# Kernel optimization log

Hardware: AMD Instinct MI355X
Metric: run time of the kernel (lower is better)

The kernel has to match this reference:

```python
import jax, jax.numpy as jnp
import numpy as np

EPS_LN = 1e-12
EPS_COS = 1e-8
B, L, H, S = 64, 512, 768, 32


def _layernorm(x, gamma, beta):
    mu = jnp.mean(x, axis=-1, keepdims=True)
    var = jnp.mean(jnp.square(x - mu), axis=-1, keepdims=True)
    return (x - mu) * jax.lax.rsqrt(var + EPS_LN) * gamma + beta


def setup_inputs() -> dict:
    key = jax.random.key(0)
    k = jax.random.split(key, 8)
    hidden_states = jax.random.normal(k[0], (B, L, H), dtype=jnp.float32)
    glyph_pooled = jax.random.normal(k[1], (B * S, H), dtype=jnp.float32)
    W = jax.random.normal(k[2], (H, H), dtype=jnp.float32) * (1.0 / np.sqrt(H))
    b = jnp.zeros((H,), dtype=jnp.float32)
    g1 = jnp.ones((H,), dtype=jnp.float32)
    b1 = jnp.zeros((H,), dtype=jnp.float32)
    g2 = jnp.ones((H,), dtype=jnp.float32)
    b2 = jnp.zeros((H,), dtype=jnp.float32)
    start = jax.random.randint(k[3], (B,), 0, 256, dtype=jnp.int64 if jax.config.jax_enable_x64 else jnp.int32)
    length = jax.random.randint(k[4], (B,), 1, 129, dtype=start.dtype)
    end = jnp.minimum(start + length, L)
    return {"hidden_states": hidden_states, "glyph_pooled": glyph_pooled, "W": W, "b": b,
            "g1": g1, "b1": b1, "g2": g2, "b2": b2, "glyph_start": start, "glyph_end": end}


def reference(hidden_states, glyph_pooled, W, b, g1, b1, g2, b2, glyph_start, glyph_end):
    # transform: Linear + LayerNorm on pooled glyph encoder output, then (b s) h -> b s h
    t = glyph_pooled @ W.T + b                         # [B*S, H]
    glyph_out = _layernorm(t, g1, b1).reshape(B, S, H)  # [B, S, H]

    # ragged mean pooling: mean over hidden_states[i, start[i]:end[i]] via mask
    pos = jnp.arange(L)[None, :]                        # [1, L]
    mask = (pos >= glyph_start[:, None]) & (pos < glyph_end[:, None])  # [B, L]
    maskf = mask.astype(hidden_states.dtype)
    count = jnp.maximum(jnp.sum(maskf, axis=1, keepdims=True), 1.0)    # [B, 1]
    seg_mean = jnp.einsum('bl,blh->bh', maskf, hidden_states) / count  # [B, H]

    sel = _layernorm(seg_mean, g2, b2)[:, None, :]      # [B, 1, H], broadcast over S

    # cosine similarity along last dim (torch default eps=1e-8)
    num = jnp.sum(sel * glyph_out, axis=-1)             # [B, S]
    nx = jnp.linalg.norm(sel, axis=-1)                  # [B, 1]
    ny = jnp.linalg.norm(glyph_out, axis=-1)            # [B, S]
    score = num / jnp.maximum(nx * ny, EPS_COS)
    return score
```

## Files before the change

kernel.cpp:

```cpp
#include <hip/hip_runtime.h>
#include <hip/hip_bf16.h>
#include <math.h>

#define BB 64
#define LL 512
#define HH 768
#define SS 32
#define MM 2048
#define EPS_LN 1e-12f
#define EPS_COS 1e-8f

#define NKS 12
#define NGB 384
#define CH_PER_G (NKS * 2 * 64)
#define A_RG (MM / 16)
#define B_RG (HH / 16)
#define LDST 772
#define SEG_SLICES 8
#define SEG_BLK (BB * SEG_SLICES)

#define SCALE_X 4096.0f
#define SCALE_W 131072.0f
#define INV_SC  1.8626451e-9f

typedef __attribute__((ext_vector_type(4))) int int4v;
typedef __attribute__((ext_vector_type(4))) float f32x4;

static __device__ inline void quant(float x, float scale,
                                    signed char& hi, signed char& lo) {
    int v = (int)rintf(x * scale);
    v = max(-32639, min(32639, v));
    const signed char l8 = (signed char)(v & 0xFF);
    hi = (signed char)((v - (int)l8) >> 8);
    lo = l8;
}

__global__ __launch_bounds__(256) void k_prep(
    const float* __restrict__ gp, const float* __restrict__ Wm,
    const float* __restrict__ hs,
    const int* __restrict__ gstart, const int* __restrict__ gend,
    int4v* __restrict__ a_ws, int4v* __restrict__ b_ws,
    float* __restrict__ pp)
{
    __shared__ __align__(16) float xs[16][LDST];
    const int bid = blockIdx.x;
    const int t = threadIdx.x;

    if (bid < SEG_BLK) {
        const int b = bid >> 3;
        const int sl = bid & 7;
        const int s0 = gstart[b], e0 = gend[b];
        const int lo = max(s0, sl * 64);
        const int hi = min(e0, sl * 64 + 64);
        const float* base = hs + (size_t)b * LL * HH;
        const int c0 = t, c1 = t + 256, c2 = t + 512;
        float a[3][4];
#pragma unroll
        for (int j = 0; j < 3; ++j)
#pragma unroll
            for (int u = 0; u < 4; ++u) a[j][u] = 0.f;
        int l = lo;
        for (; l + 4 <= hi; l += 4) {
#pragma unroll
            for (int u = 0; u < 4; ++u) {
                const float* row = base + (size_t)(l + u) * HH;
                a[0][u] += row[c0]; a[1][u] += row[c1]; a[2][u] += row[c2];
            }
        }
        for (; l < hi; ++l) {
            const float* row = base + (size_t)l * HH;
            a[0][0] += row[c0]; a[1][0] += row[c1]; a[2][0] += row[c2];
        }
        float* dst = pp + (size_t)bid * HH;
        dst[c0] = (a[0][0] + a[0][1]) + (a[0][2] + a[0][3]);
        dst[c1] = (a[1][0] + a[1][1]) + (a[1][2] + a[1][3]);
        dst[c2] = (a[2][0] + a[2][1]) + (a[2][2] + a[2][3]);
    } else {
        const bool isA = bid < SEG_BLK + A_RG;
        const int rg = isA ? (bid - SEG_BLK) : (bid - SEG_BLK - A_RG);
        const float* src = (isA ? gp : Wm) + (size_t)rg * 16 * HH;
        int4v* dst = isA ? a_ws : b_ws;
        const float sc = isA ? SCALE_X : SCALE_W;

#pragma unroll
        for (int j = 0; j < 12; ++j) {
            const int idx = t + j * 256;
            const int row = idx / 192;
            const int col = (idx - row * 192) * 4;
            *(float4*)&xs[row][col] = *(const float4*)(src + (size_t)idx * 4);
        }
        __syncthreads();

        const int l = t & 63;
        const int cslot = t >> 6;
        const int row = l & 15;
        const int koff = (l >> 4) * 16;
#pragma unroll
        for (int i = 0; i < 3; ++i) {
            const int ks = i * 4 + cslot;
            const int kbase = ks * 64 + koff;
            union { signed char c[16]; int4v v; } Hc, Lc;
#pragma unroll
            for (int q = 0; q < 4; ++q) {
                const float4 xv = *(const float4*)&xs[row][kbase + 4 * q];
                quant(xv.x, sc, Hc.c[4 * q + 0], Lc.c[4 * q + 0]);
                quant(xv.y, sc, Hc.c[4 * q + 1], Lc.c[4 * q + 1]);
                quant(xv.z, sc, Hc.c[4 * q + 2], Lc.c[4 * q + 2]);
                quant(xv.w, sc, Hc.c[4 * q + 3], Lc.c[4 * q + 3]);
            }
            dst[(size_t)(rg * NKS + ks) * 128 + l]      = Hc.v;
            dst[(size_t)(rg * NKS + ks) * 128 + 64 + l] = Lc.v;
        }
    }
}

#define TRIO(MI, NI, AH_, AL_, BH_, BL_) \
    accH[MI][NI] = __builtin_amdgcn_mfma_i32_16x16x64_i8(AH_, BH_, accH[MI][NI], 0, 0, 0); \
    accM[MI][NI] = __builtin_amdgcn_mfma_i32_16x16x64_i8(AH_, BL_, accM[MI][NI], 0, 0, 0); \
    accM[MI][NI] = __builtin_amdgcn_mfma_i32_16x16x64_i8(AL_, BH_, accM[MI][NI], 0, 0, 0);

#define DECLSET(P) int4v P##a0h,P##a0l,P##a1h,P##a1l, \
    P##b0h,P##b0l,P##b1h,P##b1l,P##b2h,P##b2l,P##b3h,P##b3l;

#define LOADSET(P, KS) { const int o_ = (KS) * 128; \
    P##a0h = ba0[o_]; P##a0l = ba0[o_ + 64]; P##a1h = ba1[o_]; P##a1l = ba1[o_ + 64]; \
    P##b0h = bb0[o_]; P##b0l = bb0[o_ + 64]; P##b1h = bb1[o_]; P##b1l = bb1[o_ + 64]; \
    P##b2h = bb2[o_]; P##b2l = bb2[o_ + 64]; P##b3h = bb3[o_]; P##b3l = bb3[o_ + 64]; }

#define MFMASET(P) \
    TRIO(0, 0, P##a0h, P##a0l, P##b0h, P##b0l) \
    TRIO(0, 1, P##a0h, P##a0l, P##b1h, P##b1l) \
    TRIO(0, 2, P##a0h, P##a0l, P##b2h, P##b2l) \
    TRIO(0, 3, P##a0h, P##a0l, P##b3h, P##b3l) \
    TRIO(1, 0, P##a1h, P##a1l, P##b0h, P##b0l) \
    TRIO(1, 1, P##a1h, P##a1l, P##b1h, P##b1l) \
    TRIO(1, 2, P##a1h, P##a1l, P##b2h, P##b2l) \
    TRIO(1, 3, P##a1h, P##a1l, P##b3h, P##b3l)

__global__ __launch_bounds__(128) void k_gemm(
    const int4v* __restrict__ aw, const int4v* __restrict__ bw,
    const float* __restrict__ pp,
    const float* __restrict__ g2, const float* __restrict__ b2,
    const int* __restrict__ gstart, const int* __restrict__ gend,
    float* __restrict__ tbuf, float* __restrict__ sel, float* __restrict__ selnorm)
{
    __shared__ float red[2][2], red2[2], sh2[2];

    if (blockIdx.x < NGB) {
        const int orig = blockIdx.x;
        const int bid = (orig & 7) * 48 + (orig >> 3);
        const int mb = bid / 12;
        const int nb = bid - mb * 12;
        const int wave = threadIdx.x >> 6;
        const int lane = threadIdx.x & 63;

        const int mg0 = mb * 4 + wave * 2;
        const int4v* ba0 = aw + (size_t)mg0 * CH_PER_G + lane;
        const int4v* ba1 = ba0 + CH_PER_G;
        const int4v* bb0 = bw + (size_t)(nb * 4) * CH_PER_G + lane;
        const int4v* bb1 = bb0 + CH_PER_G;
        const int4v* bb2 = bb1 + CH_PER_G;
        const int4v* bb3 = bb2 + CH_PER_G;

        int4v accH[2][4] = {};
        int4v accM[2][4] = {};
        DECLSET(A) DECLSET(C)

        LOADSET(A, 0)
        for (int ks = 0; ks < NKS - 2; ks += 2) {
            LOADSET(C, ks + 1)
            MFMASET(A)
            LOADSET(A, ks + 2)
            MFMASET(C)
        }
        LOADSET(C, NKS - 1)
        MFMASET(A)
        MFMASET(C)

        const int wm = mg0 * 16;
        const int wn = nb * 64;
        const int r0 = (lane >> 4) * 4;
        const int cc = lane & 15;
#pragma unroll
        for (int mi = 0; mi < 2; ++mi)
#pragma unroll
            for (int ni = 0; ni < 4; ++ni)
#pragma unroll
                for (int j = 0; j < 4; ++j) {
                    const float tv = ((float)accH[mi][ni][j] * 65536.0f
                                    + (float)accM[mi][ni][j] * 256.0f) * INV_SC;
                    tbuf[(size_t)(wm + mi * 16 + r0 + j) * HH + wn + ni * 16 + cc] = tv;
                }
    } else {
        const int cb = blockIdx.x - NGB;
        const int t = threadIdx.x;
        const int lane = t & 63, wv = t >> 6;
        const int s0 = gstart[cb], e0 = gend[cb];
        const float inv = 1.0f / fmaxf((float)(e0 - s0), 1.0f);

        float v[6];
#pragma unroll
        for (int j = 0; j < 6; ++j) v[j] = 0.f;
        const float* base = pp + (size_t)cb * SEG_SLICES * HH;
#pragma unroll
        for (int sl = 0; sl < SEG_SLICES; ++sl) {
#pragma unroll
            for (int j = 0; j < 6; ++j)
                v[j] += base[(size_t)sl * HH + t + 128 * j];
        }
        float s = 0.f, q = 0.f;
#pragma unroll
        for (int j = 0; j < 6; ++j) {
            v[j] *= inv;
            s += v[j];
            q = fmaf(v[j], v[j], q);
        }
        for (int o = 32; o > 0; o >>= 1) {
            s += __shfl_xor(s, o, 64);
            q += __shfl_xor(q, o, 64);
        }
        if (lane == 0) { red[0][wv] = s; red[1][wv] = q; }
        __syncthreads();
        if (t == 0) {
            const float ts = red[0][0] + red[0][1];
            const float tq = red[1][0] + red[1][1];
            const float mu = ts / (float)HH;
            const float var = tq / (float)HH - mu * mu;
            sh2[0] = mu;
            sh2[1] = rsqrtf(var + EPS_LN);
        }
        __syncthreads();
        const float mu = sh2[0], rinv = sh2[1];
        float n = 0.f;
#pragma unroll
        for (int j = 0; j < 6; ++j) {
            const int c = t + 128 * j;
            const float y = (v[j] - mu) * rinv * g2[c] + b2[c];
            sel[(size_t)cb * HH + c] = y;
            n = fmaf(y, y, n);
        }
        for (int o = 32; o > 0; o >>= 1) n += __shfl_xor(n, o, 64);
        if (lane == 0) red2[wv] = n;
        __syncthreads();
        if (t == 0) selnorm[cb] = sqrtf(red2[0] + red2[1]);
    }
}

__global__ __launch_bounds__(512) void k_finish(
    const float* __restrict__ tbuf, const float* __restrict__ bias,
    const float* __restrict__ g1, const float* __restrict__ b1,
    const float* __restrict__ sel, const float* __restrict__ selnorm,
    float* __restrict__ out)
{
    const int lane = threadIdx.x & 63;
    const int w = threadIdx.x >> 6;
    const int m = blockIdx.x * 8 + w;
    const int b = m >> 5;
    const float* trow = tbuf + (size_t)m * HH;

    float v[12];
#pragma unroll
    for (int j = 0; j < 12; ++j) {
        const int col = lane + 64 * j;
        v[j] = trow[col] + bias[col];
    }
    float s = 0.f, q = 0.f;
#pragma unroll
    for (int j = 0; j < 12; ++j) { s += v[j]; q = fmaf(v[j], v[j], q); }
    for (int o = 32; o > 0; o >>= 1) {
        s += __shfl_xor(s, o, 64);
        q += __shfl_xor(q, o, 64);
    }
    const float mu = s * (1.0f / (float)HH);
    const float var = q * (1.0f / (float)HH) - mu * mu;
    const float rinv = rsqrtf(var + EPS_LN);

    const float* selb = sel + (size_t)b * HH;
    float d = 0.f, n2 = 0.f;
#pragma unroll
    for (int j = 0; j < 12; ++j) {
        const int col = lane + 64 * j;
        const float y = (v[j] - mu) * rinv * g1[col] + b1[col];
        d = fmaf(y, selb[col], d);
        n2 = fmaf(y, y, n2);
    }
    for (int o = 32; o > 0; o >>= 1) {
        d += __shfl_xor(d, o, 64);
        n2 += __shfl_xor(n2, o, 64);
    }
    if (lane == 0)
        out[m] = d / fmaxf(selnorm[b] * sqrtf(n2), EPS_COS);
}

extern "C" void kernel_launch(void* const* d_in, const int* in_sizes, int n_in,
                              void* d_out, int out_size, void* d_ws, size_t ws_size,
                              hipStream_t stream) {
    const float* hs  = (const float*)d_in[0];
    const float* gp  = (const float*)d_in[1];
    const float* W   = (const float*)d_in[2];
    const float* bia = (const float*)d_in[3];
    const float* g1  = (const float*)d_in[4];
    const float* b1  = (const float*)d_in[5];
    const float* g2  = (const float*)d_in[6];
    const float* b2  = (const float*)d_in[7];
    const int* gs    = (const int*)d_in[8];
    const int* ge    = (const int*)d_in[9];
    float* out = (float*)d_out;

    char* ws = (char*)d_ws;
    int4v* a_ws  = (int4v*)ws;
    int4v* b_ws  = (int4v*)(ws + (size_t)A_RG * CH_PER_G * 16);
    float* pp      = (float*)(ws + (size_t)(A_RG + B_RG) * CH_PER_G * 16);
    float* sel     = pp + (size_t)BB * SEG_SLICES * HH;
    float* selnorm = sel + (size_t)BB * HH;
    float* tbuf    = selnorm + BB;

    k_prep<<<SEG_BLK + A_RG + B_RG, 256, 0, stream>>>(gp, W, hs, gs, ge,
                                                      a_ws, b_ws, pp);
    k_gemm<<<NGB + BB, 128, 0, stream>>>(a_ws, b_ws, pp, g2, b2, gs, ge,
                                         tbuf, sel, selnorm);
    k_finish<<<MM / 8, 512, 0, stream>>>(tbuf, bia, g1, b1, sel, selnorm, out);
}
```

Before: 28.18 us.

## Split GEMM K-loop across wave pairs with LDS reduction, reorder prep blocks, vectorize finish

The GEMM block grows from 2 to 4 waves, and each pair of waves splits the 12 K-steps in half. Partial int32 accumulators are exchanged through shared memory so that each wave finalizes one 16-row tile. This halves the serial MFMA chain per wave and adds more waves in flight, at the cost of extra LDS traffic and a block barrier. The prep kernel now schedules the quantization blocks before the segment-sum blocks, and the finish kernel uses float4 loads.

```diff
diff --git a/kernel.cpp b/kernel.cpp
--- a/kernel.cpp
+++ b/kernel.cpp
@@ -24,7 +24,6 @@
 #define INV_SC  1.8626451e-9f
 
 typedef __attribute__((ext_vector_type(4))) int int4v;
-typedef __attribute__((ext_vector_type(4))) float f32x4;
 
 static __device__ inline void quant(float x, float scale,
                                     signed char& hi, signed char& lo) {
@@ -46,9 +45,46 @@
     const int bid = blockIdx.x;
     const int t = threadIdx.x;
 
-    if (bid < SEG_BLK) {
-        const int b = bid >> 3;
-        const int sl = bid & 7;
+    if (bid < A_RG + B_RG) {
+        const bool isA = bid < A_RG;
+        const int rg = isA ? bid : (bid - A_RG);
+        const float* src = (isA ? gp : Wm) + (size_t)rg * 16 * HH;
+        int4v* dst = isA ? a_ws : b_ws;
+        const float sc = isA ? SCALE_X : SCALE_W;
+
+#pragma unroll
+        for (int j = 0; j < 12; ++j) {
+            const int idx = t + j * 256;
+            const int row = idx / 192;
+            const int col = (idx - row * 192) * 4;
+            *(float4*)&xs[row][col] = *(const float4*)(src + (size_t)idx * 4);
+        }
+        __syncthreads();
+
+        const int l = t & 63;
+        const int cslot = t >> 6;
+        const int row = l & 15;
+        const int koff = (l >> 4) * 16;
+#pragma unroll
+        for (int i = 0; i < 3; ++i) {
+            const int ks = i * 4 + cslot;
+            const int kbase = ks * 64 + koff;
+            union { signed char c[16]; int4v v; } Hc, Lc;
+#pragma unroll
+            for (int q = 0; q < 4; ++q) {
+                const float4 xv = *(const float4*)&xs[row][kbase + 4 * q];
+                quant(xv.x, sc, Hc.c[4 * q + 0], Lc.c[4 * q + 0]);
+                quant(xv.y, sc, Hc.c[4 * q + 1], Lc.c[4 * q + 1]);
+                quant(xv.z, sc, Hc.c[4 * q + 2], Lc.c[4 * q + 2]);
+                quant(xv.w, sc, Hc.c[4 * q + 3], Lc.c[4 * q + 3]);
+            }
+            dst[(size_t)(rg * NKS + ks) * 128 + l]      = Hc.v;
+            dst[(size_t)(rg * NKS + ks) * 128 + 64 + l] = Lc.v;
+        }
+    } else {
+        const int id = bid - (A_RG + B_RG);
+        const int b = id >> 3;
+        const int sl = id & 7;
         const int s0 = gstart[b], e0 = gend[b];
         const int lo = max(s0, sl * 64);
         const int hi = min(e0, sl * 64 + 64);
@@ -71,46 +107,10 @@
             const float* row = base + (size_t)l * HH;
             a[0][0] += row[c0]; a[1][0] += row[c1]; a[2][0] += row[c2];
         }
-        float* dst = pp + (size_t)bid * HH;
+        float* dst = pp + (size_t)id * HH;
         dst[c0] = (a[0][0] + a[0][1]) + (a[0][2] + a[0][3]);
         dst[c1] = (a[1][0] + a[1][1]) + (a[1][2] + a[1][3]);
         dst[c2] = (a[2][0] + a[2][1]) + (a[2][2] + a[2][3]);
-    } else {
-        const bool isA = bid < SEG_BLK + A_RG;
-        const int rg = isA ? (bid - SEG_BLK) : (bid - SEG_BLK - A_RG);
-        const float* src = (isA ? gp : Wm) + (size_t)rg * 16 * HH;
-        int4v* dst = isA ? a_ws : b_ws;
-        const float sc = isA ? SCALE_X : SCALE_W;
-
-#pragma unroll
-        for (int j = 0; j < 12; ++j) {
-            const int idx = t + j * 256;
-            const int row = idx / 192;
-            const int col = (idx - row * 192) * 4;
-            *(float4*)&xs[row][col] = *(const float4*)(src + (size_t)idx * 4);
-        }
-        __syncthreads();
-
-        const int l = t & 63;
-        const int cslot = t >> 6;
-        const int row = l & 15;
-        const int koff = (l >> 4) * 16;
-#pragma unroll
-        for (int i = 0; i < 3; ++i) {
-            const int ks = i * 4 + cslot;
-            const int kbase = ks * 64 + koff;
-            union { signed char c[16]; int4v v; } Hc, Lc;
-#pragma unroll
-            for (int q = 0; q < 4; ++q) {
-                const float4 xv = *(const float4*)&xs[row][kbase + 4 * q];
-                quant(xv.x, sc, Hc.c[4 * q + 0], Lc.c[4 * q + 0]);
-                quant(xv.y, sc, Hc.c[4 * q + 1], Lc.c[4 * q + 1]);
-                quant(xv.z, sc, Hc.c[4 * q + 2], Lc.c[4 * q + 2]);
-                quant(xv.w, sc, Hc.c[4 * q + 3], Lc.c[4 * q + 3]);
-            }
-            dst[(size_t)(rg * NKS + ks) * 128 + l]      = Hc.v;
-            dst[(size_t)(rg * NKS + ks) * 128 + 64 + l] = Lc.v;
-        }
     }
 }
 
@@ -137,14 +137,15 @@
     TRIO(1, 2, P##a1h, P##a1l, P##b2h, P##b2l) \
     TRIO(1, 3, P##a1h, P##a1l, P##b3h, P##b3l)
 
-__global__ __launch_bounds__(128) void k_gemm(
+__global__ __launch_bounds__(256) void k_gemm(
     const int4v* __restrict__ aw, const int4v* __restrict__ bw,
     const float* __restrict__ pp,
     const float* __restrict__ g2, const float* __restrict__ b2,
     const int* __restrict__ gstart, const int* __restrict__ gend,
     float* __restrict__ tbuf, float* __restrict__ sel, float* __restrict__ selnorm)
 {
-    __shared__ float red[2][2], red2[2], sh2[2];
+    __shared__ int ldsx[2][2][64 * 36];
+    __shared__ float red[2][4], red2[4], sh2[2];
 
     if (blockIdx.x < NGB) {
         const int orig = blockIdx.x;
@@ -152,9 +153,11 @@
         const int mb = bid / 12;
         const int nb = bid - mb * 12;
         const int wave = threadIdx.x >> 6;
+        const int p = wave >> 1;
+        const int kw = wave & 1;
         const int lane = threadIdx.x & 63;
 
-        const int mg0 = mb * 4 + wave * 2;
+        const int mg0 = mb * 4 + p * 2;
         const int4v* ba0 = aw + (size_t)mg0 * CH_PER_G + lane;
         const int4v* ba1 = ba0 + CH_PER_G;
         const int4v* bb0 = bw + (size_t)(nb * 4) * CH_PER_G + lane;
@@ -166,31 +169,50 @@
         int4v accM[2][4] = {};
         DECLSET(A) DECLSET(C)
 
-        LOADSET(A, 0)
-        for (int ks = 0; ks < NKS - 2; ks += 2) {
-            LOADSET(C, ks + 1)
+        const int ko = kw * 6;
+        LOADSET(A, ko + 0)
+        for (int ks = 0; ks < 4; ks += 2) {
+            LOADSET(C, ko + ks + 1)
             MFMASET(A)
-            LOADSET(A, ks + 2)
+            LOADSET(A, ko + ks + 2)
             MFMASET(C)
         }
-        LOADSET(C, NKS - 1)
+        LOADSET(C, ko + 5)
         MFMASET(A)
         MFMASET(C)
 
-        const int wm = mg0 * 16;
+        {
+            const int mi_w = 1 - kw;
+            int4v* slot = (int4v*)&ldsx[p][kw][lane * 36];
+#pragma unroll
+            for (int ni = 0; ni < 4; ++ni) {
+                slot[ni]     = accH[mi_w][ni];
+                slot[4 + ni] = accM[mi_w][ni];
+            }
+        }
+        __syncthreads();
+        int4v hfin[4], mfin[4];
+        {
+            const int4v* pslot = (const int4v*)&ldsx[p][1 - kw][lane * 36];
+#pragma unroll
+            for (int ni = 0; ni < 4; ++ni) {
+                hfin[ni] = accH[kw][ni] + pslot[ni];
+                mfin[ni] = accM[kw][ni] + pslot[4 + ni];
+            }
+        }
+
+        const int wm = (mg0 + kw) * 16;
         const int wn = nb * 64;
         const int r0 = (lane >> 4) * 4;
         const int cc = lane & 15;
 #pragma unroll
-        for (int mi = 0; mi < 2; ++mi)
-#pragma unroll
-            for (int ni = 0; ni < 4; ++ni)
-#pragma unroll
-                for (int j = 0; j < 4; ++j) {
-                    const float tv = ((float)accH[mi][ni][j] * 65536.0f
-                                    + (float)accM[mi][ni][j] * 256.0f) * INV_SC;
-                    tbuf[(size_t)(wm + mi * 16 + r0 + j) * HH + wn + ni * 16 + cc] = tv;
-                }
+        for (int ni = 0; ni < 4; ++ni)
+#pragma unroll
+            for (int j = 0; j < 4; ++j) {
+                const float tv = ((float)hfin[ni][j] * 65536.0f
+                                + (float)mfin[ni][j] * 256.0f) * INV_SC;
+                tbuf[(size_t)(wm + r0 + j) * HH + wn + ni * 16 + cc] = tv;
+            }
     } else {
         const int cb = blockIdx.x - NGB;
         const int t = threadIdx.x;
@@ -198,19 +220,19 @@
         const int s0 = gstart[cb], e0 = gend[cb];
         const float inv = 1.0f / fmaxf((float)(e0 - s0), 1.0f);
 
-        float v[6];
-#pragma unroll
-        for (int j = 0; j < 6; ++j) v[j] = 0.f;
+        float v[3];
+#pragma unroll
+        for (int j = 0; j < 3; ++j) v[j] = 0.f;
         const float* base = pp + (size_t)cb * SEG_SLICES * HH;
 #pragma unroll
         for (int sl = 0; sl < SEG_SLICES; ++sl) {
 #pragma unroll
-            for (int j = 0; j < 6; ++j)
-                v[j] += base[(size_t)sl * HH + t + 128 * j];
+            for (int j = 0; j < 3; ++j)
+                v[j] += base[(size_t)sl * HH + t + 256 * j];
         }
         float s = 0.f, q = 0.f;
 #pragma unroll
-        for (int j = 0; j < 6; ++j) {
+        for (int j = 0; j < 3; ++j) {
             v[j] *= inv;
             s += v[j];
             q = fmaf(v[j], v[j], q);
@@ -222,8 +244,8 @@
         if (lane == 0) { red[0][wv] = s; red[1][wv] = q; }
         __syncthreads();
         if (t == 0) {
-            const float ts = red[0][0] + red[0][1];
-            const float tq = red[1][0] + red[1][1];
+            const float ts = red[0][0] + red[0][1] + red[0][2] + red[0][3];
+            const float tq = red[1][0] + red[1][1] + red[1][2] + red[1][3];
             const float mu = ts / (float)HH;
             const float var = tq / (float)HH - mu * mu;
             sh2[0] = mu;
@@ -233,8 +255,8 @@
         const float mu = sh2[0], rinv = sh2[1];
         float n = 0.f;
 #pragma unroll
-        for (int j = 0; j < 6; ++j) {
-            const int c = t + 128 * j;
+        for (int j = 0; j < 3; ++j) {
+            const int c = t + 256 * j;
             const float y = (v[j] - mu) * rinv * g2[c] + b2[c];
             sel[(size_t)cb * HH + c] = y;
             n = fmaf(y, y, n);
@@ -242,7 +264,7 @@
         for (int o = 32; o > 0; o >>= 1) n += __shfl_xor(n, o, 64);
         if (lane == 0) red2[wv] = n;
         __syncthreads();
-        if (t == 0) selnorm[cb] = sqrtf(red2[0] + red2[1]);
+        if (t == 0) selnorm[cb] = sqrtf(red2[0] + red2[1] + red2[2] + red2[3]);
     }
 }
 
@@ -256,17 +278,25 @@
     const int w = threadIdx.x >> 6;
     const int m = blockIdx.x * 8 + w;
     const int b = m >> 5;
-    const float* trow = tbuf + (size_t)m * HH;
-
-    float v[12];
-#pragma unroll
-    for (int j = 0; j < 12; ++j) {
-        const int col = lane + 64 * j;
-        v[j] = trow[col] + bias[col];
-    }
+    const float4* t4  = (const float4*)(tbuf + (size_t)m * HH);
+    const float4* bi4 = (const float4*)bias;
+    const float4* g14 = (const float4*)g1;
+    const float4* b14 = (const float4*)b1;
+    const float4* s4  = (const float4*)(sel + (size_t)b * HH);
+
+    float4 v4[3];
     float s = 0.f, q = 0.f;
 #pragma unroll
-    for (int j = 0; j < 12; ++j) { s += v[j]; q = fmaf(v[j], v[j], q); }
+    for (int j = 0; j < 3; ++j) {
+        const int idx = lane + 64 * j;
+        const float4 a = t4[idx];
+        const float4 bb = bi4[idx];
+        v4[j].x = a.x + bb.x; v4[j].y = a.y + bb.y;
+        v4[j].z = a.z + bb.z; v4[j].w = a.w + bb.w;
+        s += (v4[j].x + v4[j].y) + (v4[j].z + v4[j].w);
+        q = fmaf(v4[j].x, v4[j].x, q); q = fmaf(v4[j].y, v4[j].y, q);
+        q = fmaf(v4[j].z, v4[j].z, q); q = fmaf(v4[j].w, v4[j].w, q);
+    }
     for (int o = 32; o > 0; o >>= 1) {
         s += __shfl_xor(s, o, 64);
         q += __shfl_xor(q, o, 64);
@@ -275,14 +305,18 @@
     const float var = q * (1.0f / (float)HH) - mu * mu;
     const float rinv = rsqrtf(var + EPS_LN);
 
-    const float* selb = sel + (size_t)b * HH;
     float d = 0.f, n2 = 0.f;
 #pragma unroll
-    for (int j = 0; j < 12; ++j) {
-        const int col = lane + 64 * j;
-        const float y = (v[j] - mu) * rinv * g1[col] + b1[col];
-        d = fmaf(y, selb[col], d);
-        n2 = fmaf(y, y, n2);
+    for (int j = 0; j < 3; ++j) {
+        const int idx = lane + 64 * j;
+        const float4 g = g14[idx];
+        const float4 be = b14[idx];
+        const float4 se = s4[idx];
+        float y;
+        y = (v4[j].x - mu) * rinv * g.x + be.x; d = fmaf(y, se.x, d); n2 = fmaf(y, y, n2);
+        y = (v4[j].y - mu) * rinv * g.y + be.y; d = fmaf(y, se.y, d); n2 = fmaf(y, y, n2);
+        y = (v4[j].z - mu) * rinv * g.z + be.z; d = fmaf(y, se.z, d); n2 = fmaf(y, y, n2);
+        y = (v4[j].w - mu) * rinv * g.w + be.w; d = fmaf(y, se.w, d); n2 = fmaf(y, y, n2);
     }
     for (int o = 32; o > 0; o >>= 1) {
         d += __shfl_xor(d, o, 64);
@@ -315,9 +349,9 @@
     float* selnorm = sel + (size_t)BB * HH;
     float* tbuf    = selnorm + BB;
 
-    k_prep<<<SEG_BLK + A_RG + B_RG, 256, 0, stream>>>(gp, W, hs, gs, ge,
+    k_prep<<<A_RG + B_RG + SEG_BLK, 256, 0, stream>>>(gp, W, hs, gs, ge,
                                                       a_ws, b_ws, pp);
-    k_gemm<<<NGB + BB, 128, 0, stream>>>(a_ws, b_ws, pp, g2, b2, gs, ge,
+    k_gemm<<<NGB + BB, 256, 0, stream>>>(a_ws, b_ws, pp, g2, b2, gs, ge,
                                          tbuf, sel, selnorm);
     k_finish<<<MM / 8, 512, 0, stream>>>(tbuf, bia, g1, b1, sel, selnorm, out);
 }
```

Result: slower. 37.47 us (+33.0%).
